# Performance work log

Measured on AMD Instinct MI355X. Metric: run time of the kernel, lower is better.

The kernel has to match this reference:

```python
import jax, jax.numpy as jnp
import numpy as np

HID = 2048   # hidden_size
NH = 16      # num_heads
HD = 128     # head_dim
R = 16       # compression_ratio
WIN = 128    # window_size
ROPE = HD // 2  # partial rope dim (resolve_rope_dim with use_partial_rope)
EPS = 1e-6


def rmsnorm(x, w):
    return x * jax.lax.rsqrt(jnp.mean(x * x, axis=-1, keepdims=True) + EPS) * w


def apply_rope(x, pos):
    # x: [..., S, D]; rotate first ROPE dims, pass the rest through.
    half = ROPE // 2
    inv_freq = 1.0 / (10000.0 ** (jnp.arange(half, dtype=jnp.float32) * 2.0 / ROPE))
    ang = pos.astype(jnp.float32)[:, None] * inv_freq[None, :]   # [S, half]
    cos, sin = jnp.cos(ang), jnp.sin(ang)
    x1, x2, rest = x[..., :half], x[..., half:ROPE], x[..., ROPE:]
    return jnp.concatenate([x1 * cos - x2 * sin, x1 * sin + x2 * cos, rest], axis=-1)


def setup_inputs() -> dict:
    key = jax.random.key(0)
    ks = jax.random.split(key, 16)
    s = 0.02
    return {
        "hidden_states": jax.random.normal(ks[0], (1, 2048, HID), jnp.float32),
        "Wq": jax.random.normal(ks[1], (HID, NH * HD), jnp.float32) * s,
        "bq": jnp.zeros((NH * HD,), jnp.float32),
        "Wc": jax.random.normal(ks[2], (HID, 1), jnp.float32) * s,   # learned compressor scores
        "bc": jnp.zeros((1,), jnp.float32),
        "Wk": jax.random.normal(ks[3], (HID, HD), jnp.float32) * s,  # shared compressed KV head
        "bk": jnp.zeros((HD,), jnp.float32),
        "Wv": jax.random.normal(ks[4], (HID, HD), jnp.float32) * s,
        "bv": jnp.zeros((HD,), jnp.float32),
        "Wlk": jax.random.normal(ks[5], (HID, NH * HD), jnp.float32) * s,
        "blk": jnp.zeros((NH * HD,), jnp.float32),
        "Wlv": jax.random.normal(ks[6], (HID, NH * HD), jnp.float32) * s,
        "blv": jnp.zeros((NH * HD,), jnp.float32),
        "qn_w": jnp.ones((HD,), jnp.float32),
        "kn_w": jnp.ones((HD,), jnp.float32),
        "sink_k": jax.random.normal(ks[7], (NH, HD), jnp.float32) * s,
        "sink_v": jax.random.normal(ks[8], (NH, HD), jnp.float32) * s,
        "Wo": jax.random.normal(ks[9], (NH * HD, HID), jnp.float32) * s,
        "bo": jnp.zeros((HID,), jnp.float32),
    }


def reference(hidden_states, Wq, bq, Wc, bc, Wk, bk, Wv, bv, Wlk, blk, Wlv, blv,
              qn_w, kn_w, sink_k, sink_v, Wo, bo):
    B, S, _ = hidden_states.shape
    pos = jnp.arange(S)
    scale = 1.0 / jnp.sqrt(jnp.float32(HD))

    # queries: proj -> heads -> RMSNorm -> partial RoPE
    q = (hidden_states @ Wq + bq).reshape(B, S, NH, HD).transpose(0, 2, 1, 3)  # [B,NH,S,HD]
    q = apply_rope(rmsnorm(q, qn_w), pos)

    # learned weighted KV compression: softmax over each block of R tokens
    C = S // R
    w = jax.nn.softmax((hidden_states @ Wc + bc).reshape(B, C, R), axis=-1)   # [B,C,R]
    entries = jnp.einsum('bcr,bcrh->bch', w, hidden_states.reshape(B, C, R, HID))
    block_ends = jnp.arange(C) * R + (R - 1)

    ck = apply_rope(rmsnorm(entries @ Wk + bk, kn_w), block_ends)  # [B,C,HD] (shared head)
    cv = entries @ Wv + bv                                         # [B,C,HD]

    # dense attention over compressed entries + learnable sink slot
    cs = jnp.einsum('bhsd,bcd->bhsc', q, ck) * scale               # [B,NH,S,C]
    cmask = block_ends[None, :] <= pos[:, None]                    # block fully in past
    cs = jnp.where(cmask, cs, -1e9)
    sink_s = jnp.einsum('bhsd,hd->bhs', q, sink_k) * scale         # sink always attendable
    attn = jax.nn.softmax(jnp.concatenate([cs, sink_s[..., None]], axis=-1), axis=-1)
    ctx_c = (jnp.einsum('bhsc,bcd->bhsd', attn[..., :C], cv)
             + attn[..., C:] * sink_v[None, :, None, :])

    # local sliding-window attention branch
    lk = (hidden_states @ Wlk + blk).reshape(B, S, NH, HD).transpose(0, 2, 1, 3)
    lk = apply_rope(rmsnorm(lk, kn_w), pos)
    lv = (hidden_states @ Wlv + blv).reshape(B, S, NH, HD).transpose(0, 2, 1, 3)
    ls = jnp.einsum('bhsd,bhtd->bhst', q, lk) * scale
    d = pos[:, None] - pos[None, :]
    lmask = (d >= 0) & (d <= WIN)
    lattn = jax.nn.softmax(jnp.where(lmask, ls, -1e9), axis=-1)
    ctx_l = jnp.einsum('bhst,bhtd->bhsd', lattn, lv)

    merged = 0.5 * (ctx_c + ctx_l)                                 # mean over 2 branches
    out = merged.transpose(0, 2, 1, 3).reshape(B, S, NH * HD) @ Wo + bo
    return out
```

## Files before the change

kernel.cpp:

```cpp
#include <hip/hip_runtime.h>


typedef unsigned short u16;
typedef __attribute__((ext_vector_type(8))) short short8;
typedef __attribute__((ext_vector_type(4))) float f32x4;

#define S_LEN 2048
#define HIDN  2048
#define NHEAD 16
#define HDIM  128
#define NCHNK 128
#define NKT   32
#define SCALE 0.08838834764831845f

__device__ __forceinline__ float bf2f(u16 h) {
  return __uint_as_float(((unsigned)h) << 16);
}
__device__ __forceinline__ u16 f2bf(float f) {
  unsigned u = __float_as_uint(f);
  unsigned r = (u + 0x7fffu + ((u >> 16) & 1u)) >> 16;
  return (u16)r;
}

typedef __attribute__((address_space(3))) unsigned int lds_uint;
typedef __attribute__((address_space(1))) unsigned int glb_uint;
__device__ __forceinline__ void gl_lds16(const void* g, void* l) {
  __builtin_amdgcn_global_load_lds((glb_uint*)(unsigned long long)g,
                                   (lds_uint*)(unsigned)(unsigned long long)l,
                                   16, 0, 0);
}

__global__ __launch_bounds__(256) void k_pre(
    const float* __restrict__ Wq, const float* __restrict__ Wlk, const float* __restrict__ Wlv,
    const float* __restrict__ Wo, const float* __restrict__ hs,
    const float* __restrict__ Wc, const float* __restrict__ bc,
    const float* __restrict__ Wk, const float* __restrict__ Wv,
    u16* __restrict__ Wt3, u16* __restrict__ Wt_o, u16* __restrict__ hs_bf,
    float* __restrict__ rope_c, float* __restrict__ rope_s,
    u16* __restrict__ entries_bf, u16* __restrict__ Wkv_t) {
  __shared__ float tile[32][33];
  int z = blockIdx.z;
  int tx = threadIdx.x, ty = threadIdx.y;
  int tid = ty * 32 + tx;
  if (z < 4) {
    const float* src = (z == 0) ? Wq : (z == 1) ? Wlk : (z == 2) ? Wlv : Wo;
    u16* dst = (z < 3) ? (Wt3 + (size_t)z * HIDN * HIDN) : Wt_o;
    int k0 = blockIdx.x * 32, n0 = blockIdx.y * 32;
    #pragma unroll
    for (int i = 0; i < 32; i += 8)
      tile[ty + i][tx] = src[(size_t)(k0 + ty + i) * HIDN + (n0 + tx)];
    __syncthreads();
    #pragma unroll
    for (int i = 0; i < 32; i += 8)
      dst[(size_t)(n0 + ty + i) * HIDN + (k0 + tx)] = f2bf(tile[tx][ty + i]);
    return;
  }
  int bid = blockIdx.y * 64 + blockIdx.x;
  if (z == 4) {
    size_t i4 = ((size_t)bid * 256 + tid) * 4;
    float4 v = *(const float4*)&hs[i4];
    ushort4 o;
    o.x = f2bf(v.x); o.y = f2bf(v.y); o.z = f2bf(v.z); o.w = f2bf(v.w);
    *(ushort4*)&hs_bf[i4] = o;
    return;
  }
  if (bid < 256) {
    int i = bid * 256 + tid;
    int pos = i >> 5, f = i & 31;
    float inv = __expf(-(float)f * (9.210340371976184f / 32.0f));
    float ang = (float)pos * inv;
    rope_c[i] = cosf(ang);
    rope_s[i] = sinf(ang);
    return;
  }
  if (bid < 384) {
    __shared__ float red[16][17];
    __shared__ float wgt[16];
    int c = bid - 256;
    int row = tid >> 4, seg = tid & 15;
    const float* hrow = hs + ((size_t)c * 16 + row) * HIDN;
    float p = 0.f;
    #pragma unroll 8
    for (int k = seg * 128; k < seg * 128 + 128; k += 4) {
      float4 hv = *(const float4*)&hrow[k];
      float4 wv = *(const float4*)&Wc[k];
      p += hv.x * wv.x + hv.y * wv.y + hv.z * wv.z + hv.w * wv.w;
    }
    red[row][seg] = p;
    __syncthreads();
    if (tid < 16) {
      float lg = 0.f;
      #pragma unroll
      for (int j = 0; j < 16; ++j) lg += red[tid][j];
      lg += bc[0];
      float m = lg;
      #pragma unroll
      for (int msk = 1; msk <= 8; msk <<= 1) m = fmaxf(m, __shfl_xor(m, msk));
      float ev = __expf(lg - m);
      float sum = ev;
      #pragma unroll
      for (int msk = 1; msk <= 8; msk <<= 1) sum += __shfl_xor(sum, msk);
      wgt[tid] = ev / sum;
    }
    __syncthreads();
    #pragma unroll
    for (int j = 0; j < 8; ++j) {
      int hb = tid + j * 256;
      float acc = 0.f;
      #pragma unroll
      for (int r = 0; r < 16; ++r)
        acc += wgt[r] * hs[((size_t)c * 16 + r) * HIDN + hb];
      entries_bf[(size_t)c * HIDN + hb] = f2bf(acc);
    }
    return;
  }
  if (bid < 896) {
    int idx = bid - 384;
    int zw = idx >> 8, byw = (idx >> 6) & 3, bxw = idx & 63;
    const float* src = zw ? Wv : Wk;
    u16* dst = Wkv_t + (size_t)zw * HDIM * 2048;
    int k0 = bxw * 32, n0 = byw * 32;
    #pragma unroll
    for (int i = 0; i < 32; i += 8)
      tile[ty + i][tx] = src[(size_t)(k0 + ty + i) * HDIM + (n0 + tx)];
    __syncthreads();
    #pragma unroll
    for (int i = 0; i < 32; i += 8)
      dst[(size_t)(n0 + ty + i) * 2048 + (k0 + tx)] = f2bf(tile[tx][ty + i]);
  }
}

__global__ __launch_bounds__(512, 2) void k_gemm256(
    const u16* __restrict__ A, const u16* __restrict__ Wt3,
    const u16* __restrict__ entries_bf, const u16* __restrict__ Wkv_t,
    const float* __restrict__ bq, const float* __restrict__ blk, const float* __restrict__ blv,
    const float* __restrict__ bk, const float* __restrict__ bv,
    const float* __restrict__ qn_w, const float* __restrict__ kn_w,
    const float* __restrict__ rc, const float* __restrict__ rs,
    u16* __restrict__ q_out, u16* __restrict__ lk_out, u16* __restrict__ lv_t,
    u16* __restrict__ ck_bf, u16* __restrict__ cv_t) {
  __shared__ __align__(16) u16 lds[65536];
  __shared__ float psq[2][4][128];
  int tid = threadIdx.x, lane = tid & 63;
  int wid = tid >> 6;
  int wr = wid >> 2, wc = wid & 3;
  int lin = blockIdx.x;
  int row0, col0, mode;
  const u16 *Ag, *Bg;
  if (lin < 192) {
    int swz = (lin & 7) * 24 + (lin >> 3);
    mode = swz >> 6;
    int tile = swz & 63;
    row0 = (tile & 7) * 256;
    col0 = (tile >> 3) * 256;
    Ag = A; Bg = Wt3 + (size_t)mode * HIDN * HIDN;
  } else {
    mode = 3; row0 = 0; col0 = 0;
    Ag = entries_bf; Bg = Wkv_t;
  }
  int rA = lane & 15, kg = lane >> 4;
  int srow = tid >> 3, sslot = tid & 7;
  int ssl = sslot ^ (srow & 7);

  f32x4 acc[8][4];
  #pragma unroll
  for (int m = 0; m < 8; ++m)
    #pragma unroll
    for (int n = 0; n < 4; ++n) acc[m][n] = (f32x4){0.f, 0.f, 0.f, 0.f};

  auto stage = [&](int b, int i, int kt) {
    const u16* src = (i < 4) ? Ag : Bg;
    int rg = ((i < 4) ? row0 : col0) + ((i & 3) * 64) + srow;
    gl_lds16(&src[(size_t)rg * HIDN + kt * 64 + ssl * 8],
             &lds[b * 32768 + i * 4096 + tid * 8]);
  };
  auto rdA = [&](int b, int m, int ks) -> short8 {
    int r = wr * 128 + m * 16 + rA;
    int slot = (ks * 4 + kg) ^ (r & 7);
    return *(const short8*)&lds[b * 32768 + r * 64 + slot * 8];
  };
  auto rdB = [&](int b, int n, int ks) -> short8 {
    int r = wc * 64 + n * 16 + rA;
    int slot = (ks * 4 + kg) ^ (r & 7);
    return *(const short8*)&lds[b * 32768 + 16384 + r * 64 + slot * 8];
  };

  #pragma unroll
  for (int i = 0; i < 8; ++i) stage(0, i, 0);

  short8 Af[4], Bf[4][2];
  for (int u = 0; u < NKT; ++u) {
    int cur = u & 1;
    asm volatile("s_waitcnt vmcnt(0)" ::: "memory");
    __builtin_amdgcn_sched_barrier(0);
    __builtin_amdgcn_s_barrier();
    if (u + 1 < NKT) {
      #pragma unroll
      for (int i = 0; i < 8; ++i) stage(cur ^ 1, i, u + 1);
    }
    #pragma unroll
    for (int n = 0; n < 4; ++n) { Bf[n][0] = rdB(cur, n, 0); Bf[n][1] = rdB(cur, n, 1); }
    #pragma unroll
    for (int m = 0; m < 4; ++m) Af[m] = rdA(cur, m, 0);
    asm volatile("s_waitcnt lgkmcnt(0)" ::: "memory");
    __builtin_amdgcn_sched_barrier(0);
    __builtin_amdgcn_s_setprio(1);
    #pragma unroll
    for (int m = 0; m < 4; ++m)
      #pragma unroll
      for (int n = 0; n < 4; ++n)
        acc[m][n] = __builtin_amdgcn_mfma_f32_16x16x32_bf16(Af[m], Bf[n][0], acc[m][n], 0, 0, 0);
    __builtin_amdgcn_s_setprio(0);
    #pragma unroll
    for (int m = 0; m < 4; ++m) Af[m] = rdA(cur, m, 1);
    asm volatile("s_waitcnt lgkmcnt(0)" ::: "memory");
    __builtin_amdgcn_sched_barrier(0);
    __builtin_amdgcn_s_setprio(1);
    #pragma unroll
    for (int m = 0; m < 4; ++m)
      #pragma unroll
      for (int n = 0; n < 4; ++n)
        acc[m][n] = __builtin_amdgcn_mfma_f32_16x16x32_bf16(Af[m], Bf[n][1], acc[m][n], 0, 0, 0);
    __builtin_amdgcn_s_setprio(0);
    #pragma unroll
    for (int m = 0; m < 4; ++m) Af[m] = rdA(cur, m + 4, 0);
    asm volatile("s_waitcnt lgkmcnt(0)" ::: "memory");
    __builtin_amdgcn_sched_barrier(0);
    __builtin_amdgcn_s_setprio(1);
    #pragma unroll
    for (int m = 0; m < 4; ++m)
      #pragma unroll
      for (int n = 0; n < 4; ++n)
        acc[m + 4][n] = __builtin_amdgcn_mfma_f32_16x16x32_bf16(Af[m], Bf[n][0], acc[m + 4][n], 0, 0, 0);
    __builtin_amdgcn_s_setprio(0);
    #pragma unroll
    for (int m = 0; m < 4; ++m) Af[m] = rdA(cur, m + 4, 1);
    asm volatile("s_waitcnt lgkmcnt(0)" ::: "memory");
    __builtin_amdgcn_sched_barrier(0);
    __builtin_amdgcn_s_setprio(1);
    #pragma unroll
    for (int m = 0; m < 4; ++m)
      #pragma unroll
      for (int n = 0; n < 4; ++n)
        acc[m + 4][n] = __builtin_amdgcn_mfma_f32_16x16x32_bf16(Af[m], Bf[n][1], acc[m + 4][n], 0, 0, 0);
    __builtin_amdgcn_s_setprio(0);
  }

  int cl = rA, rbase = kg * 4;
  #pragma unroll
  for (int n = 0; n < 4; ++n) {
    int dl = wc * 64 + n * 16 + cl;
    float bb;
    if (mode == 3)      bb = (dl < 128) ? bk[dl] : bv[dl - 128];
    else if (mode == 0) bb = bq[col0 + dl];
    else if (mode == 1) bb = blk[col0 + dl];
    else                bb = blv[col0 + dl];
    #pragma unroll
    for (int m = 0; m < 8; ++m)
      #pragma unroll
      for (int j = 0; j < 4; ++j) acc[m][n][j] += bb;
  }

  if (mode == 2) {
    int hh = (col0 >> 7) + (wc >> 1);
    #pragma unroll
    for (int m = 0; m < 8; ++m) {
      int sb = row0 + wr * 128 + m * 16 + rbase;
      #pragma unroll
      for (int n = 0; n < 4; ++n) {
        int dl = (wc & 1) * 64 + n * 16 + cl;
        ushort4 o;
        o.x = f2bf(acc[m][n][0]);
        o.y = f2bf(acc[m][n][1]);
        o.z = f2bf(acc[m][n][2]);
        o.w = f2bf(acc[m][n][3]);
        *(ushort4*)&lv_t[((size_t)hh * HDIM + dl) * S_LEN + sb] = o;
      }
    }
    return;
  }

  bool is_cv = (mode == 3) && (wc >= 2);
  if (!is_cv) {
    #pragma unroll
    for (int m = 0; m < 8; ++m)
      #pragma unroll
      for (int j = 0; j < 4; ++j) {
        float s2 = acc[m][0][j] * acc[m][0][j] + acc[m][1][j] * acc[m][1][j]
                 + acc[m][2][j] * acc[m][2][j] + acc[m][3][j] * acc[m][3][j];
        s2 += __shfl_xor(s2, 1); s2 += __shfl_xor(s2, 2);
        s2 += __shfl_xor(s2, 4); s2 += __shfl_xor(s2, 8);
        if (cl == 0) psq[wr][wc][m * 16 + rbase + j] = s2;
      }
  }
  __syncthreads();
  if (is_cv) {
    if (wr == 0) {
      #pragma unroll
      for (int m = 0; m < 8; ++m) {
        int cchunk = m * 16 + rbase;
        #pragma unroll
        for (int n = 0; n < 4; ++n) {
          int d = (wc - 2) * 64 + n * 16 + cl;
          #pragma unroll
          for (int j = 0; j < 4; ++j)
            cv_t[(size_t)d * NCHNK + cchunk + j] = f2bf(acc[m][n][j]);
        }
      }
    }
    return;
  }
  {
    const float* nw = (mode == 0) ? qn_w : kn_w;
    int hgrp = wc >> 1;
    float nwv[4];
    #pragma unroll
    for (int n = 0; n < 4; ++n) nwv[n] = nw[(wc & 1) * 64 + n * 16 + cl];
    #pragma unroll
    for (int m = 0; m < 8; ++m)
      #pragma unroll
      for (int j = 0; j < 4; ++j) {
        int r16 = m * 16 + rbase + j;
        int s = row0 + wr * 128 + r16;
        bool valid = (mode != 3) || (s < NCHNK);
        int sc2 = valid ? s : 0;
        int pos = (mode == 3) ? (sc2 * 16 + 15) : sc2;
        float rr2 = rsqrtf((psq[wr][hgrp * 2][r16] + psq[wr][hgrp * 2 + 1][r16]) * (1.f / 128.f) + 1e-6f);
        float o[4];
        if ((wc & 1) == 0) {
          #pragma unroll
          for (int n = 0; n < 2; ++n) {
            int i = n * 16 + cl;
            float ca = rc[pos * 32 + i], sa = rs[pos * 32 + i];
            float y1 = acc[m][n][j] * rr2 * nwv[n];
            float y2 = acc[m][n + 2][j] * rr2 * nwv[n + 2];
            o[n] = y1 * ca - y2 * sa;
            o[n + 2] = y1 * sa + y2 * ca;
          }
        } else {
          #pragma unroll
          for (int n = 0; n < 4; ++n) o[n] = acc[m][n][j] * rr2 * nwv[n];
        }
        if (valid) {
          u16* dst;
          if (mode == 3) dst = ck_bf + (size_t)s * HDIM + (wc & 1) * 64;
          else {
            u16* dstb = (mode == 0) ? q_out : lk_out;
            dst = dstb + ((size_t)((col0 >> 7) + hgrp) * S_LEN + s) * HDIM + (wc & 1) * 64;
          }
          #pragma unroll
          for (int n = 0; n < 4; ++n) dst[n * 16 + cl] = f2bf(o[n]);
        }
      }
  }
}

__global__ __launch_bounds__(256) void k_gemm_out(const u16* __restrict__ A, const u16* __restrict__ Bt,
                                                  const float* __restrict__ bias, float* __restrict__ C) {
  __shared__ __align__(16) u16 As[128 * 32];
  __shared__ __align__(16) u16 Bs[128 * 32];
  int tid = threadIdx.x, lane = tid & 63, wave = tid >> 6;
  int wr = wave >> 1, wc = wave & 1;
  int lin = blockIdx.x + (blockIdx.y << 4);
  int swz = (lin & 7) * 32 + (lin >> 3);
  int row0 = (swz & 15) * 128, col0 = (swz >> 4) * 128;
  f32x4 acc[4][4];
  #pragma unroll
  for (int m = 0; m < 4; ++m)
    #pragma unroll
    for (int n = 0; n < 4; ++n) acc[m][n] = (f32x4){0.f, 0.f, 0.f, 0.f};
  int r0 = tid >> 2, koff = (tid & 3) * 8;
  int rA = lane & 15, kg = (lane >> 4) * 8;
  for (int k0 = 0; k0 < HIDN; k0 += 32) {
    gl_lds16(&A [(size_t)(row0 + r0)      * HIDN + k0 + koff], &As[tid * 8]);
    gl_lds16(&A [(size_t)(row0 + 64 + r0) * HIDN + k0 + koff], &As[2048 + tid * 8]);
    gl_lds16(&Bt[(size_t)(col0 + r0)      * HIDN + k0 + koff], &Bs[tid * 8]);
    gl_lds16(&Bt[(size_t)(col0 + 64 + r0) * HIDN + k0 + koff], &Bs[2048 + tid * 8]);
    __syncthreads();
    short8 af[4], bfv[4];
    #pragma unroll
    for (int m = 0; m < 4; ++m) af[m]  = *(const short8*)&As[(wr * 64 + m * 16 + rA) * 32 + kg];
    #pragma unroll
    for (int n = 0; n < 4; ++n) bfv[n] = *(const short8*)&Bs[(wc * 64 + n * 16 + rA) * 32 + kg];
    #pragma unroll
    for (int m = 0; m < 4; ++m)
      #pragma unroll
      for (int n = 0; n < 4; ++n)
        acc[m][n] = __builtin_amdgcn_mfma_f32_16x16x32_bf16(af[m], bfv[n], acc[m][n], 0, 0, 0);
    __syncthreads();
  }
  int rbase = (lane >> 4) * 4, cl = lane & 15;
  #pragma unroll
  for (int m = 0; m < 4; ++m) {
    int rowb = row0 + wr * 64 + m * 16 + rbase;
    #pragma unroll
    for (int n = 0; n < 4; ++n) {
      int col = col0 + wc * 64 + n * 16 + cl;
      float bb = bias[col];
      #pragma unroll
      for (int j = 0; j < 4; ++j)
        C[(size_t)(rowb + j) * HIDN + col] = acc[m][n][j] + bb;
    }
  }
}

__global__ __launch_bounds__(256) void k_attn(const u16* __restrict__ q_bf, const u16* __restrict__ ck_bf,
                                              const u16* __restrict__ cv_t, const float* __restrict__ sink_k,
                                              const float* __restrict__ sink_v,
                                              const u16* __restrict__ lk_bf, const u16* __restrict__ lv_t,
                                              u16* __restrict__ merged) {
  __shared__ __align__(16) u16 kv[21760];
  __shared__ __align__(16) float sc[32][164];
  __shared__ __align__(16) u16 pb[32][168];
  int tid = threadIdx.x, lane = tid & 63, wave = tid >> 6;
  int lin = blockIdx.x;
  int sw = (lin & 7) * 128 + (lin >> 3);
  int s0 = (sw & 63) * 32, h = sw >> 6;
  const size_t hb = (size_t)h * S_LEN * HDIM;
  int rA = lane & 15, kg8 = (lane >> 4) * 8;
  int qt = wave & 1, wg = wave >> 1;

  short8 aq[4];
  #pragma unroll
  for (int c = 0; c < 4; ++c)
    aq[c] = *(const short8*)&q_bf[hb + (size_t)(s0 + qt * 16 + rA) * HDIM + c * 32 + kg8];

  int cmax = s0 / 16 + 2; if (cmax > 128) cmax = 128;
  int nkeys = cmax + 1;
  int nkt = (nkeys + 15) >> 4, nkc = (nkeys + 31) >> 5;

  for (int i = tid; i < cmax * 16; i += 256) {
    int r = i >> 4, cz = (i & 15) * 8;
    *(uint4*)&kv[r * 136 + cz] = *(const uint4*)&ck_bf[r * HDIM + cz];
  }
  if (tid < 128) kv[cmax * 136 + tid] = f2bf(sink_k[h * HDIM + tid]);
  __syncthreads();

  for (int kt = wg; kt < nkt; kt += 2) {
    f32x4 a = (f32x4){0.f, 0.f, 0.f, 0.f};
    #pragma unroll
    for (int c = 0; c < 4; ++c) {
      short8 bk2 = *(const short8*)&kv[(kt * 16 + rA) * 136 + c * 32 + kg8];
      a = __builtin_amdgcn_mfma_f32_16x16x32_bf16(aq[c], bk2, a, 0, 0, 0);
    }
    int rq = qt * 16 + (lane >> 4) * 4;
    #pragma unroll
    for (int j = 0; j < 4; ++j) sc[rq + j][kt * 16 + rA] = a[j];
  }
  __syncthreads();

  {
    int ql = tid >> 3, e = tid & 7, s = s0 + ql;
    int NK = nkc * 32;
    float m = -1e30f;
    for (int i = e; i < NK; i += 8) {
      if (i < nkeys) {
        float raw = sc[ql][i];
        bool valid = (i < cmax) ? (i * 16 + 15 <= s) : true;
        float v = valid ? raw * SCALE : -1e9f;
        sc[ql][i] = v;
        m = fmaxf(m, v);
      }
    }
    m = fmaxf(m, __shfl_xor(m, 1));
    m = fmaxf(m, __shfl_xor(m, 2));
    m = fmaxf(m, __shfl_xor(m, 4));
    float sum = 0.f;
    for (int i = e; i < NK; i += 8) {
      if (i < nkeys) {
        float pv = __expf(sc[ql][i] - m);
        sc[ql][i] = pv;
        sum += pv;
      }
    }
    sum += __shfl_xor(sum, 1);
    sum += __shfl_xor(sum, 2);
    sum += __shfl_xor(sum, 4);
    float inv = 1.f / sum;
    for (int i = e; i < NK; i += 8)
      pb[ql][i] = (i < nkeys) ? f2bf(sc[ql][i] * inv) : (u16)0;
  }
  __syncthreads();

  {
    int d = tid & 127, cstart = tid >> 7;
    u16 sv = f2bf(sink_v[h * HDIM + d]);
    int NC = nkc * 32;
    for (int c = cstart; c < NC; c += 2) {
      u16 v = (c < cmax) ? cv_t[(size_t)d * NCHNK + c] : ((c == cmax) ? sv : (u16)0);
      kv[d * 168 + c] = v;
    }
  }
  __syncthreads();

  f32x4 po_c[4];
  #pragma unroll
  for (int n = 0; n < 4; ++n) po_c[n] = (f32x4){0.f, 0.f, 0.f, 0.f};
  for (int kc = 0; kc < nkc; ++kc) {
    short8 pfrag = *(const short8*)&pb[qt * 16 + rA][kc * 32 + kg8];
    #pragma unroll
    for (int n = 0; n < 4; ++n) {
      short8 av = *(const short8*)&kv[(wg * 64 + n * 16 + rA) * 168 + kc * 32 + kg8];
      po_c[n] = __builtin_amdgcn_mfma_f32_16x16x32_bf16(av, pfrag, po_c[n], 0, 0, 0);
    }
  }
  __syncthreads();

  int tbase = s0 - 128;
  for (int i = tid; i < 160 * 16; i += 256) {
    int r = i >> 4, cz = (i & 15) * 8;
    int t = tbase + r;
    uint4 val = make_uint4(0, 0, 0, 0);
    if (t >= 0) val = *(const uint4*)&lk_bf[hb + (size_t)t * HDIM + cz];
    *(uint4*)&kv[r * 136 + cz] = val;
  }
  __syncthreads();

  for (int kt = wg; kt < 10; kt += 2) {
    f32x4 a = (f32x4){0.f, 0.f, 0.f, 0.f};
    #pragma unroll
    for (int c = 0; c < 4; ++c) {
      short8 bk2 = *(const short8*)&kv[(kt * 16 + rA) * 136 + c * 32 + kg8];
      a = __builtin_amdgcn_mfma_f32_16x16x32_bf16(aq[c], bk2, a, 0, 0, 0);
    }
    int rq = qt * 16 + (lane >> 4) * 4;
    #pragma unroll
    for (int j = 0; j < 4; ++j) sc[rq + j][kt * 16 + rA] = a[j];
  }
  __syncthreads();

  {
    int ql = tid >> 3, e = tid & 7;
    int ilo = 128 - s0; if (ql > ilo) ilo = ql;
    int ihi = ql + 128;
    float m = -1e30f;
    for (int i = e; i < 160; i += 8) {
      bool valid = (i >= ilo) && (i <= ihi);
      float v = valid ? sc[ql][i] * SCALE : -1e9f;
      sc[ql][i] = v;
      m = fmaxf(m, v);
    }
    m = fmaxf(m, __shfl_xor(m, 1));
    m = fmaxf(m, __shfl_xor(m, 2));
    m = fmaxf(m, __shfl_xor(m, 4));
    float sum = 0.f;
    for (int i = e; i < 160; i += 8) {
      float pv = __expf(sc[ql][i] - m);
      sc[ql][i] = pv;
      sum += pv;
    }
    sum += __shfl_xor(sum, 1);
    sum += __shfl_xor(sum, 2);
    sum += __shfl_xor(sum, 4);
    float inv = 1.f / sum;
    for (int i = e; i < 160; i += 8) pb[ql][i] = f2bf(sc[ql][i] * inv);
  }
  __syncthreads();

  {
    int d = tid & 127, c8s = tid >> 7;
    const size_t hbt = (size_t)h * HDIM * S_LEN;
    for (int c8 = c8s; c8 < 20; c8 += 2) {
      int t0 = tbase + c8 * 8;
      uint4 val = make_uint4(0, 0, 0, 0);
      if (t0 >= 0) val = *(const uint4*)&lv_t[hbt + (size_t)d * S_LEN + t0];
      *(uint4*)&kv[d * 168 + c8 * 8] = val;
    }
  }
  __syncthreads();

  {
    f32x4 po[4];
    #pragma unroll
    for (int n = 0; n < 4; ++n) po[n] = (f32x4){0.f, 0.f, 0.f, 0.f};
    #pragma unroll
    for (int kc = 0; kc < 5; ++kc) {
      short8 pfrag = *(const short8*)&pb[qt * 16 + rA][kc * 32 + kg8];
      #pragma unroll
      for (int n = 0; n < 4; ++n) {
        short8 av = *(const short8*)&kv[(wg * 64 + n * 16 + rA) * 168 + kc * 32 + kg8];
        po[n] = __builtin_amdgcn_mfma_f32_16x16x32_bf16(av, pfrag, po[n], 0, 0, 0);
      }
    }
    int q = qt * 16 + rA;
    int s = s0 + q;
    int rb = (lane >> 4) * 4;
    #pragma unroll
    for (int n = 0; n < 4; ++n) {
      int d0 = wg * 64 + n * 16 + rb;
      ushort4 o;
      o.x = f2bf(0.5f * (po[n][0] + po_c[n][0]));
      o.y = f2bf(0.5f * (po[n][1] + po_c[n][1]));
      o.z = f2bf(0.5f * (po[n][2] + po_c[n][2]));
      o.w = f2bf(0.5f * (po[n][3] + po_c[n][3]));
      *(ushort4*)&merged[(size_t)s * HIDN + h * HDIM + d0] = o;
    }
  }
}

extern "C" void kernel_launch(void* const* d_in, const int* in_sizes, int n_in,
                              void* d_out, int out_size, void* d_ws, size_t ws_size,
                              hipStream_t stream) {
  const float* hs     = (const float*)d_in[0];
  const float* Wq     = (const float*)d_in[1];
  const float* bq     = (const float*)d_in[2];
  const float* Wc     = (const float*)d_in[3];
  const float* bc     = (const float*)d_in[4];
  const float* Wk     = (const float*)d_in[5];
  const float* bk     = (const float*)d_in[6];
  const float* Wv     = (const float*)d_in[7];
  const float* bv     = (const float*)d_in[8];
  const float* Wlk    = (const float*)d_in[9];
  const float* blk    = (const float*)d_in[10];
  const float* Wlv    = (const float*)d_in[11];
  const float* blv    = (const float*)d_in[12];
  const float* qn_w   = (const float*)d_in[13];
  const float* kn_w   = (const float*)d_in[14];
  const float* sink_k = (const float*)d_in[15];
  const float* sink_v = (const float*)d_in[16];
  const float* Wo     = (const float*)d_in[17];
  const float* bo     = (const float*)d_in[18];
  float* out = (float*)d_out;

  char* p = (char*)d_ws;
  auto alloc = [&](size_t bytes) {
    char* r = p;
    p += (bytes + 255) & ~(size_t)255;
    return r;
  };
  float* rope_c  = (float*)alloc((size_t)S_LEN * 32 * 4);
  float* rope_s  = (float*)alloc((size_t)S_LEN * 32 * 4);
  u16*   hs_bf   = (u16*)  alloc((size_t)S_LEN * HIDN * 2);
  u16*   Wt3     = (u16*)  alloc((size_t)3 * HIDN * HIDN * 2);
  u16*   Wt_o    = (u16*)  alloc((size_t)HIDN * HIDN * 2);
  u16*   Wkv_t   = (u16*)  alloc((size_t)2 * HDIM * HIDN * 2);
  u16*   ent_bf  = (u16*)  alloc((size_t)256 * HIDN * 2);
  u16*   q_bf    = (u16*)  alloc((size_t)NHEAD * S_LEN * HDIM * 2);
  u16*   lk_bf   = (u16*)  alloc((size_t)NHEAD * S_LEN * HDIM * 2);
  u16*   lv_t    = (u16*)  alloc((size_t)NHEAD * HDIM * S_LEN * 2);
  u16*   ck_bf   = (u16*)  alloc((size_t)NCHNK * HDIM * 2);
  u16*   cv_t    = (u16*)  alloc((size_t)HDIM * NCHNK * 2);
  u16*   merged  = (u16*)  alloc((size_t)S_LEN * HIDN * 2);
  (void)ws_size; (void)in_sizes; (void)n_in; (void)out_size;

  k_pre<<<dim3(64, 64, 6), dim3(32, 8), 0, stream>>>(Wq, Wlk, Wlv, Wo, hs, Wc, bc, Wk, Wv,
                                                     Wt3, Wt_o, hs_bf, rope_c, rope_s,
                                                     ent_bf, Wkv_t);

  k_gemm256<<<193, 512, 0, stream>>>(hs_bf, Wt3, ent_bf, Wkv_t,
                                     bq, blk, blv, bk, bv, qn_w, kn_w,
                                     rope_c, rope_s, q_bf, lk_bf, lv_t, ck_bf, cv_t);

  k_attn<<<1024, 256, 0, stream>>>(q_bf, ck_bf, cv_t, sink_k, sink_v,
                                   lk_bf, lv_t, merged);

  k_gemm_out<<<dim3(16, 16), 256, 0, stream>>>(merged, Wt_o, bo, out);
}
```

Baseline: 224.0 us.

## Issue next-tile loads before barrier and pipeline output GEMM with swizzled LDS

In the fused projection GEMM, prefetch of the next K tile is moved ahead of the barrier. Loads are reordered so the B tile and first A half arrive first, and partial vmcnt waits let the first half of MFMAs start before the second A half lands. The output GEMM is rewritten to use the same double-buffered, XOR-swizzled 64-wide K tiles with partial waits and prioritised MFMA blocks, replacing a single-buffered load/sync loop. This adds extra barriers and relies on exact vmcnt counts matching the issue order, which is fragile.

```diff
diff --git a/kernel.cpp b/kernel.cpp
--- a/kernel.cpp
+++ b/kernel.cpp
@@ -169,10 +169,16 @@
     for (int n = 0; n < 4; ++n) acc[m][n] = (f32x4){0.f, 0.f, 0.f, 0.f};
 
   auto stage = [&](int b, int i, int kt) {
-    const u16* src = (i < 4) ? Ag : Bg;
-    int rg = ((i < 4) ? row0 : col0) + ((i & 3) * 64) + srow;
+    int ah;
+    const u16* src;
+    int rg, dofs;
+    if (i < 4) { src = Bg; rg = col0 + i * 64 + srow; dofs = 16384 + i * 4096; }
+    else {
+      ah = (i == 4) ? 0 : (i == 5) ? 2 : (i == 6) ? 1 : 3;
+      src = Ag; rg = row0 + ah * 64 + srow; dofs = ah * 4096;
+    }
     gl_lds16(&src[(size_t)rg * HIDN + kt * 64 + ssl * 8],
-             &lds[b * 32768 + i * 4096 + tid * 8]);
+             &lds[b * 32768 + dofs + tid * 8]);
   };
   auto rdA = [&](int b, int m, int ks) -> short8 {
     int r = wr * 128 + m * 16 + rA;
@@ -191,13 +197,15 @@
   short8 Af[4], Bf[4][2];
   for (int u = 0; u < NKT; ++u) {
     int cur = u & 1;
-    asm volatile("s_waitcnt vmcnt(0)" ::: "memory");
+    bool pf = (u + 1 < NKT);
+    if (pf) {
+      #pragma unroll
+      for (int i = 0; i < 8; ++i) stage(cur ^ 1, i, u + 1);
+    }
+    if (pf) asm volatile("s_waitcnt vmcnt(10)" ::: "memory");
+    else    asm volatile("s_waitcnt vmcnt(2)" ::: "memory");
     __builtin_amdgcn_sched_barrier(0);
     __builtin_amdgcn_s_barrier();
-    if (u + 1 < NKT) {
-      #pragma unroll
-      for (int i = 0; i < 8; ++i) stage(cur ^ 1, i, u + 1);
-    }
     #pragma unroll
     for (int n = 0; n < 4; ++n) { Bf[n][0] = rdB(cur, n, 0); Bf[n][1] = rdB(cur, n, 1); }
     #pragma unroll
@@ -222,6 +230,10 @@
       for (int n = 0; n < 4; ++n)
         acc[m][n] = __builtin_amdgcn_mfma_f32_16x16x32_bf16(Af[m], Bf[n][1], acc[m][n], 0, 0, 0);
     __builtin_amdgcn_s_setprio(0);
+    if (pf) asm volatile("s_waitcnt vmcnt(8)" ::: "memory");
+    else    asm volatile("s_waitcnt vmcnt(0)" ::: "memory");
+    __builtin_amdgcn_sched_barrier(0);
+    __builtin_amdgcn_s_barrier();
     #pragma unroll
     for (int m = 0; m < 4; ++m) Af[m] = rdA(cur, m + 4, 0);
     asm volatile("s_waitcnt lgkmcnt(0)" ::: "memory");
@@ -244,6 +256,7 @@
       for (int n = 0; n < 4; ++n)
         acc[m + 4][n] = __builtin_amdgcn_mfma_f32_16x16x32_bf16(Af[m], Bf[n][1], acc[m + 4][n], 0, 0, 0);
     __builtin_amdgcn_s_setprio(0);
+    __builtin_amdgcn_s_barrier();
   }
 
   int cl = rA, rbase = kg * 4;
@@ -355,41 +368,86 @@
   }
 }
 
-__global__ __launch_bounds__(256) void k_gemm_out(const u16* __restrict__ A, const u16* __restrict__ Bt,
-                                                  const float* __restrict__ bias, float* __restrict__ C) {
-  __shared__ __align__(16) u16 As[128 * 32];
-  __shared__ __align__(16) u16 Bs[128 * 32];
-  int tid = threadIdx.x, lane = tid & 63, wave = tid >> 6;
+__global__ __launch_bounds__(256, 2) void k_gemm_out(const u16* __restrict__ A, const u16* __restrict__ Bt,
+                                                     const float* __restrict__ bias, float* __restrict__ C) {
+  __shared__ __align__(16) u16 lds[32768];
+  int tid = threadIdx.x, lane = tid & 63;
+  int wave = tid >> 6;
   int wr = wave >> 1, wc = wave & 1;
   int lin = blockIdx.x + (blockIdx.y << 4);
   int swz = (lin & 7) * 32 + (lin >> 3);
   int row0 = (swz & 15) * 128, col0 = (swz >> 4) * 128;
+  int rA = lane & 15, kg = lane >> 4;
+  int srow = tid >> 3, sslot = tid & 7;
+  int ssl = sslot ^ (srow & 7);
+
   f32x4 acc[4][4];
   #pragma unroll
   for (int m = 0; m < 4; ++m)
     #pragma unroll
     for (int n = 0; n < 4; ++n) acc[m][n] = (f32x4){0.f, 0.f, 0.f, 0.f};
-  int r0 = tid >> 2, koff = (tid & 3) * 8;
-  int rA = lane & 15, kg = (lane >> 4) * 8;
-  for (int k0 = 0; k0 < HIDN; k0 += 32) {
-    gl_lds16(&A [(size_t)(row0 + r0)      * HIDN + k0 + koff], &As[tid * 8]);
-    gl_lds16(&A [(size_t)(row0 + 64 + r0) * HIDN + k0 + koff], &As[2048 + tid * 8]);
-    gl_lds16(&Bt[(size_t)(col0 + r0)      * HIDN + k0 + koff], &Bs[tid * 8]);
-    gl_lds16(&Bt[(size_t)(col0 + 64 + r0) * HIDN + k0 + koff], &Bs[2048 + tid * 8]);
-    __syncthreads();
-    short8 af[4], bfv[4];
-    #pragma unroll
-    for (int m = 0; m < 4; ++m) af[m]  = *(const short8*)&As[(wr * 64 + m * 16 + rA) * 32 + kg];
-    #pragma unroll
-    for (int n = 0; n < 4; ++n) bfv[n] = *(const short8*)&Bs[(wc * 64 + n * 16 + rA) * 32 + kg];
+
+  auto stage = [&](int b, int i, int kt) {
+    const u16* src = (i < 4) ? Bt : A;
+    int rg = ((i < 4) ? col0 : row0) + (i & 3) * 32 + srow;
+    int dofs = (i < 4) ? (8192 + i * 2048) : ((i - 4) * 2048);
+    gl_lds16(&src[(size_t)rg * HIDN + kt * 64 + ssl * 8],
+             &lds[b * 16384 + dofs + tid * 8]);
+  };
+  auto rdA = [&](int b, int m, int ks) -> short8 {
+    int r = wr * 64 + m * 16 + rA;
+    int slot = (ks * 4 + kg) ^ (r & 7);
+    return *(const short8*)&lds[b * 16384 + r * 64 + slot * 8];
+  };
+  auto rdB = [&](int b, int n, int ks) -> short8 {
+    int r = wc * 64 + n * 16 + rA;
+    int slot = (ks * 4 + kg) ^ (r & 7);
+    return *(const short8*)&lds[b * 16384 + 8192 + r * 64 + slot * 8];
+  };
+
+  #pragma unroll
+  for (int i = 0; i < 8; ++i) stage(0, i, 0);
+
+  short8 Af[4], Bf[4][2];
+  for (int u = 0; u < NKT; ++u) {
+    int cur = u & 1;
+    bool pf = (u + 1 < NKT);
+    if (pf) {
+      #pragma unroll
+      for (int i = 0; i < 8; ++i) stage(cur ^ 1, i, u + 1);
+    }
+    if (pf) asm volatile("s_waitcnt vmcnt(8)" ::: "memory");
+    else    asm volatile("s_waitcnt vmcnt(0)" ::: "memory");
+    __builtin_amdgcn_sched_barrier(0);
+    __builtin_amdgcn_s_barrier();
+    #pragma unroll
+    for (int n = 0; n < 4; ++n) { Bf[n][0] = rdB(cur, n, 0); Bf[n][1] = rdB(cur, n, 1); }
+    #pragma unroll
+    for (int m = 0; m < 4; ++m) Af[m] = rdA(cur, m, 0);
+    asm volatile("s_waitcnt lgkmcnt(0)" ::: "memory");
+    __builtin_amdgcn_sched_barrier(0);
+    __builtin_amdgcn_s_setprio(1);
     #pragma unroll
     for (int m = 0; m < 4; ++m)
       #pragma unroll
       for (int n = 0; n < 4; ++n)
-        acc[m][n] = __builtin_amdgcn_mfma_f32_16x16x32_bf16(af[m], bfv[n], acc[m][n], 0, 0, 0);
-    __syncthreads();
-  }
-  int rbase = (lane >> 4) * 4, cl = lane & 15;
+        acc[m][n] = __builtin_amdgcn_mfma_f32_16x16x32_bf16(Af[m], Bf[n][0], acc[m][n], 0, 0, 0);
+    __builtin_amdgcn_s_setprio(0);
+    #pragma unroll
+    for (int m = 0; m < 4; ++m) Af[m] = rdA(cur, m, 1);
+    asm volatile("s_waitcnt lgkmcnt(0)" ::: "memory");
+    __builtin_amdgcn_sched_barrier(0);
+    __builtin_amdgcn_s_setprio(1);
+    #pragma unroll
+    for (int m = 0; m < 4; ++m)
+      #pragma unroll
+      for (int n = 0; n < 4; ++n)
+        acc[m][n] = __builtin_amdgcn_mfma_f32_16x16x32_bf16(Af[m], Bf[n][1], acc[m][n], 0, 0, 0);
+    __builtin_amdgcn_s_setprio(0);
+    __builtin_amdgcn_s_barrier();
+  }
+
+  int rbase = kg * 4, cl = rA;
   #pragma unroll
   for (int m = 0; m < 4; ++m) {
     int rowb = row0 + wr * 64 + m * 16 + rbase;
```

After: 216.2 us. 1.04x faster.
